# Kernel tuning notes

Measured on AMD Instinct MI355X. Metric: run time of the kernel, lower is better.

Reference implementation:

```python
import jax, jax.numpy as jnp
import numpy as np

N = 50000      # nodes
E = 800000     # edges (avg degree 16)
H = 128        # hidden_dim (phi_cfg.hidden_dim)
PE = 16        # pe_dim
L = 3          # rho_cfg.num_layers
T = 32         # num_node_types
F = 8          # num_node_features (col 0 = type id, 7 continuous)
EF = 4         # num_edge_features


def setup_inputs() -> dict:
    key = jax.random.key(0)
    ks = jax.random.split(key, 16)
    p = lambda k, sh: (jax.random.normal(k, sh, jnp.float32) * 0.05)
    return {
        "x_type": jax.random.randint(ks[0], (N,), 0, T),
        "x_feat": jax.random.normal(ks[1], (N, F - 1), jnp.float32),
        "edge_index": jax.random.randint(ks[2], (2, E), 0, N),
        "edge_attr": jax.random.normal(ks[3], (E, EF), jnp.float32),
        # NodeFeatureEmbedder ('mixed' mode) params
        "type_embed": p(ks[4], (T, H)),
        "featW": p(ks[5], (F - 1, H)),
        "featb": jnp.zeros((H,), jnp.float32),
        # edge_features_embed Linear(EF -> H)
        "edgeW": p(ks[6], (EF, H)),
        "edgeb": jnp.zeros((H,), jnp.float32),
        # GIN layers: MLP per layer (H->H->H) + eps
        "W1": p(ks[7], (L, H, H)),
        "b1": jnp.zeros((L, H), jnp.float32),
        "W2": p(ks[8], (L, H, H)),
        "b2": jnp.zeros((L, H), jnp.float32),
        "eps": jnp.zeros((L,), jnp.float32),
        # final projection to pe_dim
        "Wout": p(ks[9], (H, PE)),
        "bout": jnp.zeros((PE,), jnp.float32),
    }


def reference(x_type, x_feat, edge_index, edge_attr, type_embed, featW, featb,
              edgeW, edgeb, W1, b1, W2, b2, eps, Wout, bout):
    # Node embedding: type embedding lookup + linear projection of continuous feats
    h = type_embed[x_type] + x_feat @ featW + featb          # [N, H]
    # Edge embedding
    e = edge_attr @ edgeW + edgeb                            # [E, H]
    src, dst = edge_index[0], edge_index[1]
    for l in range(L):
        # GINE message: relu(h_src + e), sum-aggregate onto destination nodes
        m = jax.nn.relu(h[src] + e)                          # [E, H] irregular gather
        agg = jax.ops.segment_sum(m, dst, num_segments=N)    # [N, H] scatter-add
        z = (1.0 + eps[l]) * h + agg
        h = jax.nn.relu(z @ W1[l] + b1[l]) @ W2[l] + b2[l]   # per-layer MLP
        h = jax.nn.relu(h)
    return h @ Wout + bout                                   # [N, PE]
```

## Files before the change

### kernel.cpp

```cpp
#include <hip/hip_runtime.h>
#include <hip/hip_bf16.h>


#define HDIM 128
#define NCH 1024
#define NPB 256

typedef unsigned int uint32;
typedef unsigned short ushort16;
typedef __attribute__((ext_vector_type(8))) short short8;
typedef __attribute__((ext_vector_type(4))) float f32x4;
typedef __attribute__((ext_vector_type(2))) float f32x2;

__device__ __forceinline__ ushort16 f2bf(float f) {
    uint32 u = __float_as_uint(f);
    u += 0x7fff + ((u >> 16) & 1);
    return (ushort16)(u >> 16);
}
__device__ __forceinline__ float bflo(uint32 g) { return __uint_as_float(g << 16); }
__device__ __forceinline__ float bfhi(uint32 g) { return __uint_as_float(g & 0xffff0000u); }

__global__ __launch_bounds__(256) void hist_kernel(const int* __restrict__ dstIdx,
                                                   int* __restrict__ histM, int E, int NB) {
    __shared__ int hist[256];
    const int b = blockIdx.x;
    for (int j = threadIdx.x; j < NB; j += 256) hist[j] = 0;
    __syncthreads();
    const int epb = (E + NCH - 1) / NCH;
    const int e0 = b * epb, e1 = min(e0 + epb, E);
    for (int e = e0 + threadIdx.x; e < e1; e += 256)
        atomicAdd(&hist[dstIdx[e] >> 8], 1);
    __syncthreads();
    for (int j = threadIdx.x; j < NB; j += 256)
        histM[j * NCH + b] = hist[j];
}

__global__ __launch_bounds__(256) void partial_kernel(const int* __restrict__ F,
                                                      int* __restrict__ partials, int M) {
    __shared__ int red[256];
    int i = blockIdx.x * 256 + threadIdx.x;
    red[threadIdx.x] = (i < M) ? F[i] : 0;
    __syncthreads();
#pragma unroll
    for (int off = 128; off > 0; off >>= 1) {
        if (threadIdx.x < off) red[threadIdx.x] += red[threadIdx.x + off];
        __syncthreads();
    }
    if (threadIdx.x == 0) partials[blockIdx.x] = red[0];
}

__global__ __launch_bounds__(1024) void scan_partials_kernel(const int* __restrict__ partials,
                                                             int* __restrict__ offsets, int nb) {
    __shared__ int buf[1024];
    int tid = threadIdx.x;
    int v0 = (tid < nb) ? partials[tid] : 0;
    buf[tid] = v0;
    __syncthreads();
#pragma unroll
    for (int off = 1; off < 1024; off <<= 1) {
        int v = (tid >= off) ? buf[tid - off] : 0;
        __syncthreads();
        buf[tid] += v;
        __syncthreads();
    }
    if (tid < nb) offsets[tid] = buf[tid] - v0;
}

__global__ __launch_bounds__(256) void excl_out_kernel(const int* __restrict__ F,
                                                       const int* __restrict__ offsets,
                                                       int* __restrict__ Fscan, int M) {
    __shared__ int buf[256];
    int tid = threadIdx.x;
    int i = blockIdx.x * 256 + tid;
    int v = (i < M) ? F[i] : 0;
    buf[tid] = v;
    __syncthreads();
#pragma unroll
    for (int off = 1; off < 256; off <<= 1) {
        int t = (tid >= off) ? buf[tid - off] : 0;
        __syncthreads();
        buf[tid] += t;
        __syncthreads();
    }
    if (i < M) Fscan[i] = buf[tid] - v + offsets[blockIdx.x];
}

__global__ __launch_bounds__(256) void chunk_scatter_kernel(
        const int* __restrict__ srcIdx, const int* __restrict__ dstIdx,
        const float* __restrict__ edge_attr, const int* __restrict__ Fscan,
        int4* __restrict__ tmp, int E, int NB) {
    __shared__ int cur[256];
    const int b = blockIdx.x;
    for (int j = threadIdx.x; j < NB; j += 256) cur[j] = Fscan[j * NCH + b];
    __syncthreads();
    const int epb = (E + NCH - 1) / NCH;
    const int e0 = b * epb, e1 = min(e0 + epb, E);
    for (int e = e0 + threadIdx.x; e < e1; e += 256) {
        int d = dstIdx[e];
        int r = atomicAdd(&cur[d >> 8], 1);
        float4 ea = *(const float4*)(edge_attr + (size_t)e * 4);
        int4 rec;
        rec.x = srcIdx[e];
        rec.y = (int)(((uint32)f2bf(ea.y) << 16) | (uint32)f2bf(ea.x));
        rec.z = (int)(((uint32)f2bf(ea.w) << 16) | (uint32)f2bf(ea.z));
        rec.w = d;
        tmp[r] = rec;
    }
}

__global__ __launch_bounds__(256) void bucket_sort_kernel(
        const int4* __restrict__ tmp, const int* __restrict__ Fscan,
        int* __restrict__ row_ptr, int4* __restrict__ adj, int E, int NB, int N) {
    __shared__ int cnt[256];
    __shared__ int cur[256];
    const int bkt = blockIdx.x;
    const int tid = threadIdx.x;
    const int base = Fscan[bkt * NCH];
    const int endb = (bkt + 1 < NB) ? Fscan[(bkt + 1) * NCH] : E;

    cnt[tid] = 0;
    __syncthreads();
    for (int i = base + tid; i < endb; i += 256)
        atomicAdd(&cnt[tmp[i].w & 255], 1);
    __syncthreads();
    int orig = cnt[tid];
#pragma unroll
    for (int off = 1; off < 256; off <<= 1) {
        int v = (tid >= off) ? cnt[tid - off] : 0;
        __syncthreads();
        cnt[tid] += v;
        __syncthreads();
    }
    int excl = cnt[tid] - orig;
    int node = bkt * NPB + tid;
    if (node <= N) row_ptr[node] = base + excl;
    cur[tid] = base + excl;
    __syncthreads();
    for (int i = base + tid; i < endb; i += 256) {
        int4 rec = tmp[i];
        int pos = atomicAdd(&cur[rec.w & 255], 1);
        adj[pos] = rec;
    }
}

__global__ void prep_weights(const float* __restrict__ W1, const float* __restrict__ W2,
                             ushort16* __restrict__ Wb1t, ushort16* __restrict__ Wb2t, int total) {
    int idx = blockIdx.x * 256 + threadIdx.x;
    if (idx >= total) return;
    int l = idx >> 14;
    int rem = idx & 16383;
    int n = rem >> 7, k = rem & 127;
    size_t src = (size_t)l * 16384 + (size_t)k * 128 + n;
    size_t dst = (size_t)l * 16384 + (size_t)n * 128 + k;
    Wb1t[dst] = f2bf(W1[src]);
    Wb2t[dst] = f2bf(W2[src]);
}

__global__ void embed_kernel(const int* __restrict__ x_type, const float* __restrict__ x_feat,
                             const float* __restrict__ type_embed, const float* __restrict__ featW,
                             const float* __restrict__ featb, ushort16* __restrict__ h, int N) {
    int idx = blockIdx.x * 256 + threadIdx.x;
    int n = idx >> 7, c = idx & 127;
    if (n >= N) return;
    int t = x_type[n];
    float acc = type_embed[(size_t)t * HDIM + c] + featb[c];
#pragma unroll
    for (int k = 0; k < 7; ++k)
        acc = fmaf(x_feat[(size_t)n * 7 + k], featW[(size_t)k * HDIM + c], acc);
    h[(size_t)n * HDIM + c] = f2bf(acc);
}

__global__ __launch_bounds__(128) void agg_kernel(
        const uint32* __restrict__ hq,
        const int* __restrict__ row_ptr,
        const int4* __restrict__ adj,
        const float* __restrict__ edgeW, const float* __restrict__ edgeb,
        const float* __restrict__ eps, int l, uint32* __restrict__ zq, int N) {
    const int node = blockIdx.x * 2 + (threadIdx.x >> 6);
    const int lane = threadIdx.x & 63;
    if (node >= N) return;
    const int c0 = 2 * lane;
    const f32x2 w0 = {edgeW[c0],       edgeW[c0 + 1]};
    const f32x2 w1 = {edgeW[128 + c0], edgeW[128 + c0 + 1]};
    const f32x2 w2 = {edgeW[256 + c0], edgeW[256 + c0 + 1]};
    const f32x2 w3 = {edgeW[384 + c0], edgeW[384 + c0 + 1]};
    const f32x2 eb = {edgeb[c0],       edgeb[c0 + 1]};

    const int beg = __builtin_amdgcn_readfirstlane(row_ptr[node]);
    const int end = __builtin_amdgcn_readfirstlane(row_ptr[node + 1]);

    const uint32 gs = hq[(size_t)node * 64 + lane];

    f32x2 accA = {0.f, 0.f}, accB = {0.f, 0.f};

#define EDGE(Q, G, ACC) {                                                     \
        f32x2 e = eb;                                                         \
        e += bflo((uint32)(Q).y) * w0;                                        \
        e += bfhi((uint32)(Q).y) * w1;                                        \
        e += bflo((uint32)(Q).z) * w2;                                        \
        e += bfhi((uint32)(Q).z) * w3;                                        \
        ACC.x += fmaxf(bflo(G) + e.x, 0.f);                                   \
        ACC.y += fmaxf(bfhi(G) + e.y, 0.f);                                   \
    }

    int i = beg;
    for (; i + 8 <= end; i += 8) {
        int4 q0 = adj[i + 0], q1 = adj[i + 1], q2 = adj[i + 2], q3 = adj[i + 3];
        int4 q4 = adj[i + 4], q5 = adj[i + 5], q6 = adj[i + 6], q7 = adj[i + 7];
        uint32 g0 = hq[(size_t)q0.x * 64 + lane];
        uint32 g1 = hq[(size_t)q1.x * 64 + lane];
        uint32 g2 = hq[(size_t)q2.x * 64 + lane];
        uint32 g3 = hq[(size_t)q3.x * 64 + lane];
        uint32 g4 = hq[(size_t)q4.x * 64 + lane];
        uint32 g5 = hq[(size_t)q5.x * 64 + lane];
        uint32 g6 = hq[(size_t)q6.x * 64 + lane];
        uint32 g7 = hq[(size_t)q7.x * 64 + lane];
        EDGE(q0, g0, accA); EDGE(q1, g1, accB);
        EDGE(q2, g2, accA); EDGE(q3, g3, accB);
        EDGE(q4, g4, accA); EDGE(q5, g5, accB);
        EDGE(q6, g6, accA); EDGE(q7, g7, accB);
    }
    for (; i + 4 <= end; i += 4) {
        int4 q0 = adj[i + 0], q1 = adj[i + 1], q2 = adj[i + 2], q3 = adj[i + 3];
        uint32 g0 = hq[(size_t)q0.x * 64 + lane];
        uint32 g1 = hq[(size_t)q1.x * 64 + lane];
        uint32 g2 = hq[(size_t)q2.x * 64 + lane];
        uint32 g3 = hq[(size_t)q3.x * 64 + lane];
        EDGE(q0, g0, accA); EDGE(q1, g1, accB);
        EDGE(q2, g2, accA); EDGE(q3, g3, accB);
    }
    for (; i < end; ++i) {
        int4 q = adj[i];
        uint32 g = hq[(size_t)q.x * 64 + lane];
        EDGE(q, g, accA);
    }
#undef EDGE

    const float ep = 1.0f + eps[l];
    float zl = fmaf(ep, bflo(gs), accA.x + accB.x);
    float zh = fmaf(ep, bfhi(gs), accA.y + accB.y);
    zq[(size_t)node * 64 + lane] = ((uint32)f2bf(zh) << 16) | (uint32)f2bf(zl);
}

#define T_STRIDE 136
__global__ __launch_bounds__(64) void mlp_mfma(
        const ushort16* __restrict__ zq,
        const ushort16* __restrict__ Wb1t,
        const float* __restrict__ b1,
        const ushort16* __restrict__ Wb2t,
        const float* __restrict__ b2,
        ushort16* __restrict__ h_out, int N) {
    __shared__ ushort16 t_lds[16 * T_STRIDE];
    const int lane = threadIdx.x & 63;
    const int c = lane & 15, g = lane >> 4;
    const int wrow0 = blockIdx.x * 16;

    const ushort16* zrow = zq + (size_t)(wrow0 + c) * HDIM + g * 8;
    short8 bf[4];
#pragma unroll
    for (int kk = 0; kk < 4; ++kk)
        bf[kk] = *(const short8*)(zrow + kk * 32);

    f32x4 acc[8];
#pragma unroll
    for (int n = 0; n < 8; ++n) {
        float4 bb = *(const float4*)(b1 + n * 16 + g * 4);
        acc[n] = (f32x4){bb.x, bb.y, bb.z, bb.w};
    }
#pragma unroll
    for (int kk = 0; kk < 4; ++kk) {
#pragma unroll
        for (int n = 0; n < 8; ++n) {
            short8 af = *(const short8*)(Wb1t + (size_t)(n * 16 + c) * HDIM + kk * 32 + g * 8);
            acc[n] = __builtin_amdgcn_mfma_f32_16x16x32_bf16(af, bf[kk], acc[n], 0, 0, 0);
        }
    }
#pragma unroll
    for (int n = 0; n < 8; ++n) {
        ushort4 u;
        u.x = f2bf(fmaxf(acc[n][0], 0.f));
        u.y = f2bf(fmaxf(acc[n][1], 0.f));
        u.z = f2bf(fmaxf(acc[n][2], 0.f));
        u.w = f2bf(fmaxf(acc[n][3], 0.f));
        *(ushort4*)(&t_lds[c * T_STRIDE + n * 16 + g * 4]) = u;
    }
    __syncthreads();

    short8 bf2[4];
#pragma unroll
    for (int kk = 0; kk < 4; ++kk)
        bf2[kk] = *(const short8*)(&t_lds[c * T_STRIDE + kk * 32 + g * 8]);

    f32x4 acc2[8];
#pragma unroll
    for (int n = 0; n < 8; ++n) {
        float4 bb = *(const float4*)(b2 + n * 16 + g * 4);
        acc2[n] = (f32x4){bb.x, bb.y, bb.z, bb.w};
    }
#pragma unroll
    for (int kk = 0; kk < 4; ++kk) {
#pragma unroll
        for (int n = 0; n < 8; ++n) {
            short8 af = *(const short8*)(Wb2t + (size_t)(n * 16 + c) * HDIM + kk * 32 + g * 8);
            acc2[n] = __builtin_amdgcn_mfma_f32_16x16x32_bf16(af, bf2[kk], acc2[n], 0, 0, 0);
        }
    }
    if (wrow0 + c < N) {
#pragma unroll
        for (int n = 0; n < 8; ++n) {
            ushort4 u;
            u.x = f2bf(fmaxf(acc2[n][0], 0.f));
            u.y = f2bf(fmaxf(acc2[n][1], 0.f));
            u.z = f2bf(fmaxf(acc2[n][2], 0.f));
            u.w = f2bf(fmaxf(acc2[n][3], 0.f));
            *(ushort4*)(h_out + (size_t)(wrow0 + c) * HDIM + n * 16 + g * 4) = u;
        }
    }
}

__global__ __launch_bounds__(256) void out_kernel(
        const uint32* __restrict__ hq, const float* __restrict__ Wout,
        const float* __restrict__ bout, float* __restrict__ out, int N) {
    __shared__ uint32 rows[16][64];
    const int tid = threadIdx.x;
    const int n0 = blockIdx.x * 16;
#pragma unroll
    for (int s = 0; s < 4; ++s) {
        int idx = tid + s * 256;
        int r = idx >> 6, cc = idx & 63;
        int n = n0 + r;
        rows[r][cc] = (n < N) ? hq[(size_t)n * 64 + cc] : 0u;
    }
    __syncthreads();
    const int r = tid >> 4, pe = tid & 15;
    const int n = n0 + r;
    if (n >= N) return;
    float acc = bout[pe];
#pragma unroll 8
    for (int k2 = 0; k2 < 64; ++k2) {
        uint32 g = rows[r][k2];
        acc = fmaf(bflo(g), Wout[(2 * k2) * 16 + pe], acc);
        acc = fmaf(bfhi(g), Wout[(2 * k2 + 1) * 16 + pe], acc);
    }
    out[(size_t)n * 16 + pe] = acc;
}

extern "C" void kernel_launch(void* const* d_in, const int* in_sizes, int n_in,
                              void* d_out, int out_size, void* d_ws, size_t ws_size,
                              hipStream_t stream) {
    const int*   x_type     = (const int*)  d_in[0];
    const float* x_feat     = (const float*)d_in[1];
    const int*   edge_index = (const int*)  d_in[2];
    const float* edge_attr  = (const float*)d_in[3];
    const float* type_embed = (const float*)d_in[4];
    const float* featW      = (const float*)d_in[5];
    const float* featb      = (const float*)d_in[6];
    const float* edgeW      = (const float*)d_in[7];
    const float* edgeb      = (const float*)d_in[8];
    const float* W1         = (const float*)d_in[9];
    const float* b1         = (const float*)d_in[10];
    const float* W2         = (const float*)d_in[11];
    const float* b2         = (const float*)d_in[12];
    const float* eps        = (const float*)d_in[13];
    const float* Wout       = (const float*)d_in[14];
    const float* bout       = (const float*)d_in[15];

    const int N = in_sizes[0];
    const int E = in_sizes[2] / 2;
    const int L = in_sizes[13];
    const int N64 = (N + 63) & ~63;
    const int NB  = (N + NPB - 1) / NPB;
    const int M   = NB * NCH;

    const int* srcIdx = edge_index;
    const int* dstIdx = edge_index + E;

    auto align256 = [](size_t x) { return (x + 255) & ~(size_t)255; };
    char* p = (char*)d_ws;
    ushort16* h_buf  = (ushort16*)p;           p += align256((size_t)N64 * HDIM * 2);
    ushort16* z_buf  = (ushort16*)p;           p += align256((size_t)N64 * HDIM * 2);
    int*   row_ptr   = (int*)p;                p += align256((size_t)(N + 1) * 4);
    int*   histM     = (int*)p;                p += align256((size_t)M * 4);
    int*   Fscan     = (int*)p;                p += align256((size_t)M * 4);
    int*   partials  = (int*)p;                p += align256(1024 * 4);
    int*   offsets   = (int*)p;                p += align256(1024 * 4);
    int4*  tmp       = (int4*)p;               p += align256((size_t)E * 16);
    int4*  adj       = (int4*)p;               p += align256((size_t)E * 16);
    ushort16* Wb1t   = (ushort16*)p;           p += align256((size_t)L * HDIM * HDIM * 2);
    ushort16* Wb2t   = (ushort16*)p;           p += align256((size_t)L * HDIM * HDIM * 2);
    (void)ws_size;

    hist_kernel<<<NCH, 256, 0, stream>>>(dstIdx, histM, E, NB);
    const int pblocks = (M + 255) / 256;
    partial_kernel<<<pblocks, 256, 0, stream>>>(histM, partials, M);
    scan_partials_kernel<<<1, 1024, 0, stream>>>(partials, offsets, pblocks);
    excl_out_kernel<<<pblocks, 256, 0, stream>>>(histM, offsets, Fscan, M);
    chunk_scatter_kernel<<<NCH, 256, 0, stream>>>(srcIdx, dstIdx, edge_attr, Fscan, tmp, E, NB);
    bucket_sort_kernel<<<NB, 256, 0, stream>>>(tmp, Fscan, row_ptr, adj, E, NB, N);

    const int wtotal = L * HDIM * HDIM;
    prep_weights<<<(wtotal + 255) / 256, 256, 0, stream>>>(W1, W2, Wb1t, Wb2t, wtotal);

    embed_kernel<<<((size_t)N * HDIM + 255) / 256, 256, 0, stream>>>(
        x_type, x_feat, type_embed, featW, featb, h_buf, N);

    const int mlp_blocks = (N + 15) / 16;
    for (int l = 0; l < L; ++l) {
        agg_kernel<<<(N + 1) / 2, 128, 0, stream>>>(
            (const uint32*)h_buf, row_ptr, adj, edgeW, edgeb, eps, l,
            (uint32*)z_buf, N);
        mlp_mfma<<<mlp_blocks, 64, 0, stream>>>(
            z_buf, Wb1t + (size_t)l * HDIM * HDIM, b1 + (size_t)l * HDIM,
            Wb2t + (size_t)l * HDIM * HDIM, b2 + (size_t)l * HDIM, h_buf, N);
    }

    out_kernel<<<(N + 15) / 16, 256, 0, stream>>>(
        (const uint32*)h_buf, Wout, bout, (float*)d_out, N);
}
```

Before: 280.3 us.

## Merge preprocessing kernels and fuse partial reduction with last-block scan

Histogram, weight conversion and node embedding now run as block ranges of one launch. The partial-sum reduction and the scan of partials are merged into one kernel, where the last block to finish (found with an atomic counter) does the scan. The exclusive scan now uses 1024-thread blocks. This cuts kernel launches and gaps between them, at the cost of a done counter that must be reset each call and a serial tail in the last block.

```diff
diff --git a/kernel.cpp b/kernel.cpp
--- a/kernel.cpp
+++ b/kernel.cpp
@@ -20,63 +20,100 @@
 __device__ __forceinline__ float bflo(uint32 g) { return __uint_as_float(g << 16); }
 __device__ __forceinline__ float bfhi(uint32 g) { return __uint_as_float(g & 0xffff0000u); }
 
-__global__ __launch_bounds__(256) void hist_kernel(const int* __restrict__ dstIdx,
-                                                   int* __restrict__ histM, int E, int NB) {
+__global__ __launch_bounds__(256) void pre_kernel(
+        const int* __restrict__ dstIdx, int* __restrict__ histM, int E, int NB,
+        const float* __restrict__ W1, const float* __restrict__ W2,
+        ushort16* __restrict__ Wb1t, ushort16* __restrict__ Wb2t, int wtotal,
+        const int* __restrict__ x_type, const float* __restrict__ x_feat,
+        const float* __restrict__ type_embed, const float* __restrict__ featW,
+        const float* __restrict__ featb, ushort16* __restrict__ h, int N,
+        int* __restrict__ done, int prepB) {
     __shared__ int hist[256];
     const int b = blockIdx.x;
-    for (int j = threadIdx.x; j < NB; j += 256) hist[j] = 0;
-    __syncthreads();
-    const int epb = (E + NCH - 1) / NCH;
-    const int e0 = b * epb, e1 = min(e0 + epb, E);
-    for (int e = e0 + threadIdx.x; e < e1; e += 256)
-        atomicAdd(&hist[dstIdx[e] >> 8], 1);
-    __syncthreads();
-    for (int j = threadIdx.x; j < NB; j += 256)
-        histM[j * NCH + b] = hist[j];
-}
-
-__global__ __launch_bounds__(256) void partial_kernel(const int* __restrict__ F,
-                                                      int* __restrict__ partials, int M) {
-    __shared__ int red[256];
-    int i = blockIdx.x * 256 + threadIdx.x;
-    red[threadIdx.x] = (i < M) ? F[i] : 0;
-    __syncthreads();
-#pragma unroll
-    for (int off = 128; off > 0; off >>= 1) {
-        if (threadIdx.x < off) red[threadIdx.x] += red[threadIdx.x + off];
-        __syncthreads();
-    }
-    if (threadIdx.x == 0) partials[blockIdx.x] = red[0];
-}
-
-__global__ __launch_bounds__(1024) void scan_partials_kernel(const int* __restrict__ partials,
-                                                             int* __restrict__ offsets, int nb) {
+    if (b == 0 && threadIdx.x == 0) *done = 0;
+
+    if (b < NCH) {
+        for (int j = threadIdx.x; j < NB; j += 256) hist[j] = 0;
+        __syncthreads();
+        const int epb = (E + NCH - 1) / NCH;
+        const int e0 = b * epb, e1 = min(e0 + epb, E);
+        for (int e = e0 + threadIdx.x; e < e1; e += 256)
+            atomicAdd(&hist[dstIdx[e] >> 8], 1);
+        __syncthreads();
+        for (int j = threadIdx.x; j < NB; j += 256)
+            histM[j * NCH + b] = hist[j];
+    } else if (b < NCH + prepB) {
+        int idx = (b - NCH) * 256 + threadIdx.x;
+        if (idx < wtotal) {
+            int l = idx >> 14;
+            int rem = idx & 16383;
+            int n = rem >> 7, k = rem & 127;
+            size_t src = (size_t)l * 16384 + (size_t)k * 128 + n;
+            size_t dst = (size_t)l * 16384 + (size_t)n * 128 + k;
+            Wb1t[dst] = f2bf(W1[src]);
+            Wb2t[dst] = f2bf(W2[src]);
+        }
+    } else {
+        int idx = (b - NCH - prepB) * 256 + threadIdx.x;
+        int n = idx >> 7, c = idx & 127;
+        if (n < N) {
+            int t = x_type[n];
+            float acc = type_embed[(size_t)t * HDIM + c] + featb[c];
+#pragma unroll
+            for (int k = 0; k < 7; ++k)
+                acc = fmaf(x_feat[(size_t)n * 7 + k], featW[(size_t)k * HDIM + c], acc);
+            h[(size_t)n * HDIM + c] = f2bf(acc);
+        }
+    }
+}
+
+__global__ __launch_bounds__(1024) void partial_scan_kernel(
+        const int* __restrict__ F, int* __restrict__ partials,
+        int* __restrict__ offsets, int* __restrict__ done, int M, int nblocks) {
+    __shared__ int red[1024];
+    __shared__ int lastFlag;
+    const int tid = threadIdx.x;
+    int i = blockIdx.x * 1024 + tid;
+    red[tid] = (i < M) ? F[i] : 0;
+    __syncthreads();
+#pragma unroll
+    for (int off = 512; off > 0; off >>= 1) {
+        if (tid < off) red[tid] += red[tid + off];
+        __syncthreads();
+    }
+    if (tid == 0) {
+        partials[blockIdx.x] = red[0];
+        __threadfence();
+        int old = atomicAdd(done, 1);
+        lastFlag = (old == nblocks - 1);
+    }
+    __syncthreads();
+    if (lastFlag) {
+        int v = (tid < nblocks) ? atomicAdd(&partials[tid], 0) : 0;
+        red[tid] = v;
+        __syncthreads();
+#pragma unroll
+        for (int off = 1; off < 1024; off <<= 1) {
+            int t = (tid >= off) ? red[tid - off] : 0;
+            __syncthreads();
+            red[tid] += t;
+            __syncthreads();
+        }
+        if (tid < nblocks) offsets[tid] = red[tid] - v;
+    }
+}
+
+__global__ __launch_bounds__(1024) void excl_out_kernel(const int* __restrict__ F,
+                                                        const int* __restrict__ offsets,
+                                                        int* __restrict__ Fscan, int M) {
     __shared__ int buf[1024];
-    int tid = threadIdx.x;
-    int v0 = (tid < nb) ? partials[tid] : 0;
-    buf[tid] = v0;
-    __syncthreads();
-#pragma unroll
-    for (int off = 1; off < 1024; off <<= 1) {
-        int v = (tid >= off) ? buf[tid - off] : 0;
-        __syncthreads();
-        buf[tid] += v;
-        __syncthreads();
-    }
-    if (tid < nb) offsets[tid] = buf[tid] - v0;
-}
-
-__global__ __launch_bounds__(256) void excl_out_kernel(const int* __restrict__ F,
-                                                       const int* __restrict__ offsets,
-                                                       int* __restrict__ Fscan, int M) {
-    __shared__ int buf[256];
-    int tid = threadIdx.x;
-    int i = blockIdx.x * 256 + tid;
+    const int tid = threadIdx.x;
+    int i = blockIdx.x * 1024 + tid;
     int v = (i < M) ? F[i] : 0;
     buf[tid] = v;
     __syncthreads();
 #pragma unroll
-    for (int off = 1; off < 256; off <<= 1) {
+    for (int off = 1; off < 1024; off <<= 1) {
         int t = (tid >= off) ? buf[tid - off] : 0;
         __syncthreads();
         buf[tid] += t;
@@ -141,33 +178,6 @@
         int pos = atomicAdd(&cur[rec.w & 255], 1);
         adj[pos] = rec;
     }
-}
-
-__global__ void prep_weights(const float* __restrict__ W1, const float* __restrict__ W2,
-                             ushort16* __restrict__ Wb1t, ushort16* __restrict__ Wb2t, int total) {
-    int idx = blockIdx.x * 256 + threadIdx.x;
-    if (idx >= total) return;
-    int l = idx >> 14;
-    int rem = idx & 16383;
-    int n = rem >> 7, k = rem & 127;
-    size_t src = (size_t)l * 16384 + (size_t)k * 128 + n;
-    size_t dst = (size_t)l * 16384 + (size_t)n * 128 + k;
-    Wb1t[dst] = f2bf(W1[src]);
-    Wb2t[dst] = f2bf(W2[src]);
-}
-
-__global__ void embed_kernel(const int* __restrict__ x_type, const float* __restrict__ x_feat,
-                             const float* __restrict__ type_embed, const float* __restrict__ featW,
-                             const float* __restrict__ featb, ushort16* __restrict__ h, int N) {
-    int idx = blockIdx.x * 256 + threadIdx.x;
-    int n = idx >> 7, c = idx & 127;
-    if (n >= N) return;
-    int t = x_type[n];
-    float acc = type_embed[(size_t)t * HDIM + c] + featb[c];
-#pragma unroll
-    for (int k = 0; k < 7; ++k)
-        acc = fmaf(x_feat[(size_t)n * 7 + k], featW[(size_t)k * HDIM + c], acc);
-    h[(size_t)n * HDIM + c] = f2bf(acc);
 }
 
 __global__ __launch_bounds__(128) void agg_kernel(
@@ -384,25 +394,28 @@
     int*   Fscan     = (int*)p;                p += align256((size_t)M * 4);
     int*   partials  = (int*)p;                p += align256(1024 * 4);
     int*   offsets   = (int*)p;                p += align256(1024 * 4);
+    int*   done      = (int*)p;                p += align256(256);
     int4*  tmp       = (int4*)p;               p += align256((size_t)E * 16);
     int4*  adj       = (int4*)p;               p += align256((size_t)E * 16);
     ushort16* Wb1t   = (ushort16*)p;           p += align256((size_t)L * HDIM * HDIM * 2);
     ushort16* Wb2t   = (ushort16*)p;           p += align256((size_t)L * HDIM * HDIM * 2);
     (void)ws_size;
 
-    hist_kernel<<<NCH, 256, 0, stream>>>(dstIdx, histM, E, NB);
-    const int pblocks = (M + 255) / 256;
-    partial_kernel<<<pblocks, 256, 0, stream>>>(histM, partials, M);
-    scan_partials_kernel<<<1, 1024, 0, stream>>>(partials, offsets, pblocks);
-    excl_out_kernel<<<pblocks, 256, 0, stream>>>(histM, offsets, Fscan, M);
+    const int wtotal = L * HDIM * HDIM;
+    const int prepB  = (wtotal + 255) / 256;
+    const int embedB = ((int)((size_t)N * HDIM) + 255) / 256;
+
+    pre_kernel<<<NCH + prepB + embedB, 256, 0, stream>>>(
+        dstIdx, histM, E, NB,
+        W1, W2, Wb1t, Wb2t, wtotal,
+        x_type, x_feat, type_embed, featW, featb, h_buf, N,
+        done, prepB);
+
+    const int pblocks = (M + 1023) / 1024;
+    partial_scan_kernel<<<pblocks, 1024, 0, stream>>>(histM, partials, offsets, done, M, pblocks);
+    excl_out_kernel<<<pblocks, 1024, 0, stream>>>(histM, offsets, Fscan, M);
     chunk_scatter_kernel<<<NCH, 256, 0, stream>>>(srcIdx, dstIdx, edge_attr, Fscan, tmp, E, NB);
     bucket_sort_kernel<<<NB, 256, 0, stream>>>(tmp, Fscan, row_ptr, adj, E, NB, N);
-
-    const int wtotal = L * HDIM * HDIM;
-    prep_weights<<<(wtotal + 255) / 256, 256, 0, stream>>>(W1, W2, Wb1t, Wb2t, wtotal);
-
-    embed_kernel<<<((size_t)N * HDIM + 255) / 256, 256, 0, stream>>>(
-        x_type, x_feat, type_embed, featW, featb, h_buf, N);
 
     const int mlp_blocks = (N + 15) / 16;
     for (int l = 0; l < L; ++l) {
```

Result: no change. 280.1 us (-0.1%).
